# Optimization experiments

Hardware: AMD Instinct MI355X
Metric: run time of the kernel (lower is better)

The kernel has to match this reference:

```python
import jax, jax.numpy as jnp
import numpy as np

N_EMBED = 1024
HIDDEN = int(2 / 3 * 4 * N_EMBED)  # 2730, matches SwiGLU default
NUM_EXPERTS = 8
TOP_K = 2


def setup_inputs() -> dict:
    key = jax.random.key(0)
    ks = jax.random.split(key, 5)
    B, T, C, E, H = 2, 2048, N_EMBED, NUM_EXPERTS, HIDDEN
    s = 0.02
    return {
        "x": jax.random.normal(ks[0], (B, T, C), dtype=jnp.float32),
        "gate_w": jax.random.normal(ks[1], (E, C), dtype=jnp.float32) * s,  # Linear(C->E) weight [out,in]
        "w1": jax.random.normal(ks[2], (E, H, C), dtype=jnp.float32) * s,   # per-expert Linear(C->H)
        "w2": jax.random.normal(ks[3], (E, H, C), dtype=jnp.float32) * s,   # per-expert Linear(C->H)
        "w3": jax.random.normal(ks[4], (E, C, H), dtype=jnp.float32) * s,   # per-expert Linear(H->C)
    }


def reference(x, gate_w, w1, w2, w3):
    B, T, C = x.shape
    E = gate_w.shape[0]
    xt = x.reshape(-1, C)                      # [N, C], N = B*T
    N = xt.shape[0]

    # Router: top-k logits, softmax over the selected logits only
    logits = jnp.einsum("nc,ec->ne", xt, gate_w)          # [N, E]
    top_vals, top_idx = jax.lax.top_k(logits, TOP_K)       # [N, K]
    top_w = jax.nn.softmax(top_vals.astype(jnp.float32), axis=-1).astype(x.dtype)

    # Dense routing-weight matrix [N, E] (top-k indices are distinct per token)
    route = jnp.zeros((N, E), dtype=x.dtype)
    route = route.at[jnp.arange(N)[:, None], top_idx].set(top_w)

    # SwiGLU for all experts, batched over the expert axis (faithful math,
    # vectorized instead of the per-expert Python-loop gather/scatter)
    h1 = jnp.einsum("nc,ehc->enh", xt, w1)                 # [E, N, H]
    h2 = jnp.einsum("nc,ehc->enh", xt, w2)                 # [E, N, H]
    act = jax.nn.silu(h1) * h2                              # [E, N, H]
    expert_out = jnp.einsum("enh,ech->enc", act, w3)       # [E, N, C]

    out = jnp.einsum("ne,enc->nc", route, expert_out)      # weighted combine
    return out.reshape(B, T, C)
```

## Files before the change

### kernel.cpp

```cpp
#include <hip/hip_runtime.h>
#include <hip/hip_bf16.h>
#include <cstdint>
#include <cstddef>

#define TOKENS 4096
#define CDIM   1024
#define HDIM   2730
#define HPAD2  2816
#define NEXP   8
#define NPAIR  (TOKENS * 2)
#define NTB1   (HPAD2 / 128)
#define NTB2   (CDIM / 128)
#define NT1    (CDIM / 64)
#define NT2    (HPAD2 / 64)

typedef __bf16 bf16_t;
typedef bf16_t bf16x8 __attribute__((ext_vector_type(8)));
typedef float  f32x4  __attribute__((ext_vector_type(4)));

static __device__ __forceinline__ unsigned short f2bf(float f) {
    union { float f; unsigned int u; } v; v.f = f;
    unsigned int u = v.u;
    return (unsigned short)((u + 0x7FFFu + ((u >> 16) & 1u)) >> 16);
}
static __device__ __forceinline__ unsigned int pack2(float a, float b) {
    return (unsigned int)f2bf(a) | ((unsigned int)f2bf(b) << 16);
}

typedef __attribute__((address_space(3))) unsigned int lds_uint;
typedef const __attribute__((address_space(1))) unsigned int glob_uint;
static __device__ __forceinline__ void gl_lds16(const void* g, void* l) {
    __builtin_amdgcn_global_load_lds((glob_uint*)g, (lds_uint*)l, 16, 0, 0);
}


__global__ __launch_bounds__(256) void moe_zero(int* meta, float* out) {
    int b = blockIdx.x;
    float4 z4 = {0.f, 0.f, 0.f, 0.f};
#pragma unroll
    for (int i = 0; i < 4; ++i)
        ((float4*)out)[(size_t)b * 1024 + i * 256 + threadIdx.x] = z4;
    if (b == 0) {
        meta[threadIdx.x] = 0;
        meta[256 + threadIdx.x] = 0;
    }
}

__global__ __launch_bounds__(256) void moe_router(
    const float* __restrict__ x, const float* __restrict__ gw,
    int* __restrict__ meta, int* __restrict__ tok_idx, float* __restrict__ tok_w)
{
    int wave = threadIdx.x >> 6;
    int lane = threadIdx.x & 63;
    int t = blockIdx.x * 4 + wave;

    float acc[NEXP];
#pragma unroll
    for (int e = 0; e < NEXP; ++e) acc[e] = 0.f;

    const float4* xr = (const float4*)(x + (size_t)t * CDIM);
#pragma unroll
    for (int it = 0; it < 4; ++it) {
        int c4 = it * 64 + lane;
        float4 xv = xr[c4];
#pragma unroll
        for (int e = 0; e < NEXP; ++e) {
            float4 gv = ((const float4*)(gw + e * CDIM))[c4];
            acc[e] += xv.x * gv.x + xv.y * gv.y + xv.z * gv.z + xv.w * gv.w;
        }
    }
#pragma unroll
    for (int e = 0; e < NEXP; ++e) {
#pragma unroll
        for (int off = 32; off > 0; off >>= 1)
            acc[e] += __shfl_xor(acc[e], off, 64);
    }
    if (lane == 0) {
        int e0 = 0; float v0 = acc[0];
#pragma unroll
        for (int e = 1; e < NEXP; ++e) if (acc[e] > v0) { v0 = acc[e]; e0 = e; }
        int e1 = -1; float v1 = -3.0e38f;
#pragma unroll
        for (int e = 0; e < NEXP; ++e) if (e != e0 && acc[e] > v1) { v1 = acc[e]; e1 = e; }
        float w0 = 1.f / (1.f + __expf(v1 - v0));
        tok_idx[2 * t] = e0; tok_idx[2 * t + 1] = e1;
        tok_w[2 * t] = w0;  tok_w[2 * t + 1] = 1.f - w0;
        atomicAdd(&meta[e0], 1);
        atomicAdd(&meta[e1], 1);
    }
}

__global__ void moe_scan(int* meta) {
    if (threadIdx.x == 0) {
        int s = 0;
        for (int e = 0; e < NEXP; ++e) { meta[8 + e] = s; s += meta[e]; }
        meta[16] = s;
        int nb1 = 0;
        for (int e = 0; e < NEXP; ++e) {
            int beg = meta[8 + e], end = meta[8 + e] + meta[e];
            for (int m0 = beg; m0 < end; m0 += 256) {
                meta[32 + 2 * nb1] = e;
                meta[33 + 2 * nb1] = m0;
                ++nb1;
            }
        }
        meta[17] = nb1;
        int nb2 = 0;
        for (int e = 0; e < NEXP; ++e) {
            int beg = meta[8 + e], end = meta[8 + e] + meta[e];
            for (int m0 = beg; m0 < end; m0 += 128) {
                meta[128 + 2 * nb2] = e;
                meta[129 + 2 * nb2] = m0;
                ++nb2;
            }
        }
        meta[20] = nb2;
    }
}

__global__ __launch_bounds__(256) void moe_scatter(
    const int* __restrict__ tok_idx, const float* __restrict__ tok_w, int* meta,
    int* __restrict__ pair_token, float* __restrict__ pair_w)
{
    int t = blockIdx.x * 256 + threadIdx.x;
    if (t >= TOKENS) return;
#pragma unroll
    for (int k = 0; k < 2; ++k) {
        int e = tok_idx[2 * t + k];
        int pos = atomicAdd(&meta[24 + e], 1);
        int slot = meta[8 + e] + pos;
        pair_token[slot] = t;
        pair_w[slot] = tok_w[2 * t + k];
    }
}

__global__ __launch_bounds__(256) void moe_gather(
    const float* __restrict__ x, const int* __restrict__ pair_token,
    unsigned short* __restrict__ Xg)
{
    int base = blockIdx.x * 8;
    int i = threadIdx.x;
#pragma unroll
    for (int r = 0; r < 8; ++r) {
        int row = base + r;
        int t = pair_token[row];
        float4 v = ((const float4*)(x + (size_t)t * CDIM))[i];
        ushort4 o;
        o.x = f2bf(v.x); o.y = f2bf(v.y); o.z = f2bf(v.z); o.w = f2bf(v.w);
        ((ushort4*)(Xg + (size_t)row * CDIM))[i] = o;
    }
}

__global__ __launch_bounds__(256) void conv_all(
    const float* __restrict__ w1, const float* __restrict__ w2, const float* __restrict__ w3,
    unsigned short* __restrict__ w1b, unsigned short* __restrict__ w2b,
    unsigned short* __restrict__ w3b)
{
    int e = blockIdx.y;
    int z = blockIdx.z;
    if (z < 2) {
        const float* wsrc = z ? w2 : w1;
        unsigned short* wdst = z ? w2b : w1b;
        int half = threadIdx.x >> 7;
        int col = (threadIdx.x & 127) * 8;
#pragma unroll
        for (int r = 0; r < 4; ++r) {
            int row = blockIdx.x * 8 + r * 2 + half;
            unsigned short* dst = wdst + ((size_t)e * HPAD2 + row) * CDIM;
            uint4 pv;
            if (row < HDIM) {
                const float* src = wsrc + ((size_t)e * HDIM + row) * CDIM + col;
                float4 a = *(const float4*)(src);
                float4 b = *(const float4*)(src + 4);
                pv.x = pack2(a.x, a.y); pv.y = pack2(a.z, a.w);
                pv.z = pack2(b.x, b.y); pv.w = pack2(b.z, b.w);
            } else {
                pv = uint4{0, 0, 0, 0};
            }
            *(uint4*)(dst + col) = pv;
        }
    } else {
        if (blockIdx.x >= CDIM / 8) return;
#pragma unroll
        for (int r = 0; r < 8; ++r) {
            int row = blockIdx.x * 8 + r;
            const float* src = w3 + ((size_t)e * CDIM + row) * HDIM;
            unsigned short* dst = w3b + ((size_t)e * CDIM + row) * HPAD2;
            for (int ch = threadIdx.x; ch < HPAD2 / 8; ch += 256) {
                int h = ch * 8;
                uint4 pv;
                if (h + 8 <= HDIM) {
                    float2 a = *(const float2*)(src + h);
                    float2 b = *(const float2*)(src + h + 2);
                    float2 c = *(const float2*)(src + h + 4);
                    float2 d = *(const float2*)(src + h + 6);
                    pv.x = pack2(a.x, a.y); pv.y = pack2(b.x, b.y);
                    pv.z = pack2(c.x, c.y); pv.w = pack2(d.x, d.y);
                } else if (h < HDIM) {
                    float v[8];
#pragma unroll
                    for (int q = 0; q < 8; ++q) v[q] = (h + q < HDIM) ? src[h + q] : 0.f;
                    pv.x = pack2(v[0], v[1]); pv.y = pack2(v[2], v[3]);
                    pv.z = pack2(v[4], v[5]); pv.w = pack2(v[6], v[7]);
                } else {
                    pv = uint4{0, 0, 0, 0};
                }
                *(uint4*)(dst + h) = pv;
            }
        }
    }
}

#define SWZ(row, ch) (((row) << 6) + ((((ch) ^ ((row) & 7))) << 3))

__global__ __launch_bounds__(512, 2) void moe_gemm1(
    const unsigned short* __restrict__ Xg,
    const unsigned short* __restrict__ w1b, const unsigned short* __restrict__ w2b,
    const float* __restrict__ pair_w, int* __restrict__ meta,
    unsigned short* __restrict__ act)
{
    __shared__ unsigned short sA[2][256 * 64];
    __shared__ unsigned short sB[2][256 * 64];
    __shared__ int sTile;

    int tid = threadIdx.x;
    int lane = tid & 63;
    int wv = tid >> 6;
    int wm = wv >> 2, wn = wv & 3;
    int l3 = lane >> 3;
    int l15 = lane & 15, l4 = lane >> 4;
    int srcc = (((lane & 7) ^ l3) << 3);

    int ntile = meta[17] * NTB1;

    for (;;) {
        if (tid == 0) sTile = atomicAdd(&meta[18], 1);
        __syncthreads();
        int t = sTile;
        if (t >= ntile) break;

        int bm = t / NTB1, bn = t - bm * NTB1;
        int e  = meta[32 + 2 * bm];
        int m0 = meta[33 + 2 * bm];
        int mEnd = meta[9 + e];
        int mEndm1 = mEnd - 1;
        int n0 = bn * 128;

        const unsigned short* w1e = w1b + (size_t)e * HPAD2 * CDIM + (size_t)n0 * CDIM;
        const unsigned short* w2e = w2b + (size_t)e * HPAD2 * CDIM + (size_t)n0 * CDIM;
        const unsigned short* bbase = (wv < 4) ? w1e : w2e;

        f32x4 acc1[8][2], acc2[8][2];
#pragma unroll
        for (int i = 0; i < 8; ++i)
#pragma unroll
            for (int j = 0; j < 2; ++j) {
                acc1[i][j] = {0.f, 0.f, 0.f, 0.f};
                acc2[i][j] = {0.f, 0.f, 0.f, 0.f};
            }

        auto STAGE_A = [&](int b, int kk) {
            int k0 = kk * 64;
#pragma unroll
            for (int i_ = 0; i_ < 4; ++i_) {
                int seg = wv * 4 + i_;
                int arow = seg * 8 + l3;
                int grow = m0 + arow; if (grow > mEndm1) grow = mEndm1;
                gl_lds16(Xg + (size_t)grow * CDIM + k0 + srcc, sA[b] + seg * 512);
            }
        };
        auto STAGE_B = [&](int b, int kk) {
            int k0 = kk * 64;
#pragma unroll
            for (int i_ = 0; i_ < 4; ++i_) {
                int seg = wv * 4 + i_;
                int bseg = (wv < 4) ? seg : seg - 16;
                gl_lds16(bbase + (size_t)(bseg * 8 + l3) * CDIM + k0 + srcc, sB[b] + seg * 512);
            }
        };

        STAGE_A(0, 0); STAGE_B(0, 0);
        STAGE_A(1, 1); STAGE_B(1, 1);
        asm volatile("s_waitcnt vmcnt(8)" ::: "memory");
        __builtin_amdgcn_s_barrier();

        for (int t_ = 0; t_ < NT1; ++t_) {
            int cur = t_ & 1;
            const unsigned short* A = sA[cur];
            const unsigned short* B = sB[cur];
            bf16x8 af[2][4], b1f[2][2], b2f[2][2];

#pragma unroll
            for (int ks = 0; ks < 2; ++ks) {
                int kch = ks * 4 + l4;
#pragma unroll
                for (int i = 0; i < 4; ++i)
                    af[ks][i] = *(const bf16x8*)(A + SWZ(wm * 128 + i * 16 + l15, kch));
#pragma unroll
                for (int j = 0; j < 2; ++j)
                    b1f[ks][j] = *(const bf16x8*)(B + SWZ(wn * 32 + j * 16 + l15, kch));
            }
            __builtin_amdgcn_s_barrier();
            asm volatile("s_waitcnt lgkmcnt(0)" ::: "memory");
            __builtin_amdgcn_s_setprio(1);
#pragma unroll
            for (int ks = 0; ks < 2; ++ks)
#pragma unroll
                for (int i = 0; i < 4; ++i)
#pragma unroll
                    for (int j = 0; j < 2; ++j)
                        acc1[i][j] = __builtin_amdgcn_mfma_f32_16x16x32_bf16(af[ks][i], b1f[ks][j], acc1[i][j], 0, 0, 0);
            __builtin_amdgcn_s_setprio(0);
            __builtin_amdgcn_s_barrier();

#pragma unroll
            for (int ks = 0; ks < 2; ++ks) {
                int kch = ks * 4 + l4;
#pragma unroll
                for (int j = 0; j < 2; ++j)
                    b2f[ks][j] = *(const bf16x8*)(B + SWZ(128 + wn * 32 + j * 16 + l15, kch));
            }
            __builtin_amdgcn_s_barrier();
            asm volatile("s_waitcnt lgkmcnt(0)" ::: "memory");
            __builtin_amdgcn_s_setprio(1);
#pragma unroll
            for (int ks = 0; ks < 2; ++ks)
#pragma unroll
                for (int i = 0; i < 4; ++i)
#pragma unroll
                    for (int j = 0; j < 2; ++j)
                        acc2[i][j] = __builtin_amdgcn_mfma_f32_16x16x32_bf16(af[ks][i], b2f[ks][j], acc2[i][j], 0, 0, 0);
            __builtin_amdgcn_s_setprio(0);
            __builtin_amdgcn_s_barrier();

#pragma unroll
            for (int ks = 0; ks < 2; ++ks) {
                int kch = ks * 4 + l4;
#pragma unroll
                for (int i = 0; i < 4; ++i)
                    af[ks][i] = *(const bf16x8*)(A + SWZ(wm * 128 + 64 + i * 16 + l15, kch));
            }
            if (t_ + 2 < NT1) STAGE_B(cur, t_ + 2);
            __builtin_amdgcn_s_barrier();
            asm volatile("s_waitcnt lgkmcnt(0)" ::: "memory");
            __builtin_amdgcn_s_setprio(1);
#pragma unroll
            for (int ks = 0; ks < 2; ++ks)
#pragma unroll
                for (int i = 0; i < 4; ++i)
#pragma unroll
                    for (int j = 0; j < 2; ++j)
                        acc1[4 + i][j] = __builtin_amdgcn_mfma_f32_16x16x32_bf16(af[ks][i], b1f[ks][j], acc1[4 + i][j], 0, 0, 0);
            __builtin_amdgcn_s_setprio(0);
            __builtin_amdgcn_s_barrier();

            if (t_ + 2 < NT1) {
                STAGE_A(cur, t_ + 2);
                asm volatile("s_waitcnt vmcnt(8)" ::: "memory");
            } else {
                asm volatile("s_waitcnt vmcnt(0)" ::: "memory");
            }
            __builtin_amdgcn_s_barrier();
            __builtin_amdgcn_s_setprio(1);
#pragma unroll
            for (int ks = 0; ks < 2; ++ks)
#pragma unroll
                for (int i = 0; i < 4; ++i)
#pragma unroll
                    for (int j = 0; j < 2; ++j)
                        acc2[4 + i][j] = __builtin_amdgcn_mfma_f32_16x16x32_bf16(af[ks][i], b2f[ks][j], acc2[4 + i][j], 0, 0, 0);
            __builtin_amdgcn_s_setprio(0);
            __builtin_amdgcn_s_barrier();
        }

#pragma unroll
        for (int i = 0; i < 8; ++i) {
            int rbase = m0 + wm * 128 + ((i & 3) * 16) + ((i >> 2) * 64) + (l4 << 2);
#pragma unroll
            for (int r = 0; r < 4; ++r) {
                int grow = rbase + r;
                if (grow >= mEnd) continue;
                float pw = pair_w[grow];
                size_t rowoff = (size_t)grow * HPAD2;
#pragma unroll
                for (int j = 0; j < 2; ++j) {
                    int gcol = n0 + wn * 32 + j * 16 + l15;
                    int ai = (i & 3) + ((i >> 2) << 2);
                    float h1 = acc1[ai][j][r], h2 = acc2[ai][j][r];
                    float a = (h1 / (1.f + __expf(-h1))) * h2 * pw;
                    act[rowoff + gcol] = f2bf(a);
                }
            }
        }
    }
}

__global__ __launch_bounds__(512, 2) void moe_gemm2(
    const unsigned short* __restrict__ act,
    const unsigned short* __restrict__ w3b,
    int* __restrict__ meta, const int* __restrict__ pair_token,
    float* __restrict__ out)
{
    __shared__ unsigned short sA[2][128 * 64];
    __shared__ unsigned short sB[2][128 * 64];
    __shared__ int sTile;

    int tid = threadIdx.x;
    int lane = tid & 63;
    int wv = tid >> 6;
    int wm = wv >> 2, wn = wv & 3;
    int l3 = lane >> 3;
    int srcc = (((lane & 7) ^ l3) << 3);

    int ntile = meta[20] * NTB2;

    for (;;) {
        if (tid == 0) sTile = atomicAdd(&meta[19], 1);
        __syncthreads();
        int t = sTile;
        if (t >= ntile) break;

        int bm = t / NTB2, bn = t - bm * NTB2;
        int e  = meta[128 + 2 * bm];
        int m0 = meta[129 + 2 * bm];
        int mEnd = meta[9 + e];
        int mEndm1 = mEnd - 1;
        int n0 = bn * 128;

        const unsigned short* w3e = w3b + (size_t)e * CDIM * HPAD2 + (size_t)n0 * HPAD2;

        f32x4 acc[4][2];
#pragma unroll
        for (int i = 0; i < 4; ++i)
#pragma unroll
            for (int j = 0; j < 2; ++j) acc[i][j] = {0.f, 0.f, 0.f, 0.f};

        auto STAGE = [&](int b, int kk) {
            int k0 = kk * 64;
#pragma unroll
            for (int i_ = 0; i_ < 2; ++i_) {
                int seg = wv * 2 + i_;
                int row = seg * 8 + l3;
                int grow = m0 + row; if (grow > mEndm1) grow = mEndm1;
                gl_lds16(act + (size_t)grow * HPAD2 + k0 + srcc, sA[b] + seg * 512);
                gl_lds16(w3e + (size_t)row * HPAD2 + k0 + srcc, sB[b] + seg * 512);
            }
        };

        STAGE(0, 0);
        __syncthreads();
        for (int t_ = 0; t_ < NT2; ++t_) {
            int cur = t_ & 1;
            if (t_ + 1 < NT2) STAGE(cur ^ 1, t_ + 1);
#pragma unroll
            for (int ks = 0; ks < 2; ++ks) {
                int kch = ks * 4 + (lane >> 4);
                bf16x8 af[4], bf[2];
#pragma unroll
                for (int i = 0; i < 4; ++i) {
                    int r = wm * 64 + i * 16 + (lane & 15);
                    af[i] = *(const bf16x8*)(sA[cur] + SWZ(r, kch));
                }
#pragma unroll
                for (int j = 0; j < 2; ++j) {
                    int r = wn * 32 + j * 16 + (lane & 15);
                    bf[j] = *(const bf16x8*)(sB[cur] + SWZ(r, kch));
                }
#pragma unroll
                for (int i = 0; i < 4; ++i)
#pragma unroll
                    for (int j = 0; j < 2; ++j)
                        acc[i][j] = __builtin_amdgcn_mfma_f32_16x16x32_bf16(af[i], bf[j], acc[i][j], 0, 0, 0);
            }
            __syncthreads();
        }

#pragma unroll
        for (int i = 0; i < 4; ++i) {
            int rbase = m0 + wm * 64 + i * 16 + ((lane >> 4) << 2);
#pragma unroll
            for (int r = 0; r < 4; ++r) {
                int grow = rbase + r;
                if (grow >= mEnd) continue;
                int tok = pair_token[grow];
                float* orow = out + (size_t)tok * CDIM;
#pragma unroll
                for (int j = 0; j < 2; ++j) {
                    int gcol = n0 + wn * 32 + j * 16 + (lane & 15);
                    atomicAdd(orow + gcol, acc[i][j][r]);
                }
            }
        }
    }
}

extern "C" void kernel_launch(void* const* d_in, const int* in_sizes, int n_in,
                              void* d_out, int out_size, void* d_ws, size_t ws_size,
                              hipStream_t stream)
{
    const float* x  = (const float*)d_in[0];
    const float* gw = (const float*)d_in[1];
    const float* w1 = (const float*)d_in[2];
    const float* w2 = (const float*)d_in[3];
    const float* w3 = (const float*)d_in[4];
    float* out = (float*)d_out;

    char* ws = (char*)d_ws;
    size_t off = 0;
    auto alloc = [&](size_t bytes) -> void* {
        off = (off + 255) & ~(size_t)255;
        void* p = ws + off;
        off += bytes;
        return p;
    };
    int*   meta       = (int*)alloc(512 * sizeof(int));
    int*   tok_idx    = (int*)alloc((size_t)NPAIR * sizeof(int));
    float* tok_w      = (float*)alloc((size_t)NPAIR * sizeof(float));
    int*   pair_token = (int*)alloc((size_t)NPAIR * sizeof(int));
    float* pair_w     = (float*)alloc((size_t)NPAIR * sizeof(float));
    unsigned short* Xg  = (unsigned short*)alloc((size_t)NPAIR * CDIM * 2);
    unsigned short* act = (unsigned short*)alloc((size_t)NPAIR * HPAD2 * 2);
    unsigned short* w1b = (unsigned short*)alloc((size_t)NEXP * HPAD2 * CDIM * 2);
    unsigned short* w2b = (unsigned short*)alloc((size_t)NEXP * HPAD2 * CDIM * 2);
    unsigned short* w3b = (unsigned short*)alloc((size_t)NEXP * CDIM * HPAD2 * 2);
    (void)ws_size; (void)in_sizes; (void)n_in; (void)out_size;

    moe_zero<<<1024, 256, 0, stream>>>(meta, out);
    moe_router<<<TOKENS / 4, 256, 0, stream>>>(x, gw, meta, tok_idx, tok_w);
    moe_scan<<<1, 64, 0, stream>>>(meta);
    moe_scatter<<<TOKENS / 256, 256, 0, stream>>>(tok_idx, tok_w, meta, pair_token, pair_w);
    moe_gather<<<NPAIR / 8, 256, 0, stream>>>(x, pair_token, Xg);
    conv_all<<<dim3(HPAD2 / 8, NEXP, 3), 256, 0, stream>>>(w1, w2, w3, w1b, w2b, w3b);
    moe_gemm1<<<256, 512, 0, stream>>>(Xg, w1b, w2b, pair_w, meta, act);
    moe_gemm2<<<512, 512, 0, stream>>>(act, w3b, meta, pair_token, out);
}
```

Before: 507.8 us.

## Fuse prep kernels, overlap w3 conversion into gemm1, split gemm2 K in halves

Folds zeroing of the output into the router launch, merges the token gather with the w1/w2 bf16 conversion, and moves the w3 conversion into the tail of gemm1's persistent tile queue. This removes several launches and their serialization. gemm2 now splits the K dimension into two halves per tile, doubling tile count to improve load balance across CUs, which relies on atomic accumulation into the output. The cost is extra atomic traffic in gemm2, and w3 conversion blocks compete with gemm1 tiles for the same workers.

```diff
diff --git a/kernel.cpp b/kernel.cpp
--- a/kernel.cpp
+++ b/kernel.cpp
@@ -12,7 +12,8 @@
 #define NTB1   (HPAD2 / 128)
 #define NTB2   (CDIM / 128)
 #define NT1    (CDIM / 64)
-#define NT2    (HPAD2 / 64)
+#define NT2H   (HPAD2 / 2 / 64)
+#define NCONV3 256
 
 typedef __bf16 bf16_t;
 typedef bf16_t bf16x8 __attribute__((ext_vector_type(8)));
@@ -34,22 +35,19 @@
 }
 
 
-__global__ __launch_bounds__(256) void moe_zero(int* meta, float* out) {
-    int b = blockIdx.x;
-    float4 z4 = {0.f, 0.f, 0.f, 0.f};
-#pragma unroll
-    for (int i = 0; i < 4; ++i)
-        ((float4*)out)[(size_t)b * 1024 + i * 256 + threadIdx.x] = z4;
-    if (b == 0) {
-        meta[threadIdx.x] = 0;
-        meta[256 + threadIdx.x] = 0;
-    }
-}
-
-__global__ __launch_bounds__(256) void moe_router(
+__global__ __launch_bounds__(256) void moe_router_zero(
     const float* __restrict__ x, const float* __restrict__ gw,
-    int* __restrict__ meta, int* __restrict__ tok_idx, float* __restrict__ tok_w)
+    int* __restrict__ meta, int* __restrict__ tok_idx, float* __restrict__ tok_w,
+    float* __restrict__ out)
 {
+    if (blockIdx.x >= 1024) {
+        int b = blockIdx.x - 1024;
+        float4 z4 = {0.f, 0.f, 0.f, 0.f};
+#pragma unroll
+        for (int i = 0; i < 4; ++i)
+            ((float4*)out)[(size_t)b * 1024 + i * 256 + threadIdx.x] = z4;
+        return;
+    }
     int wave = threadIdx.x >> 6;
     int lane = threadIdx.x & 63;
     int t = blockIdx.x * 4 + wave;
@@ -134,68 +132,99 @@
     }
 }
 
-__global__ __launch_bounds__(256) void moe_gather(
+__global__ __launch_bounds__(256) void moe_gather_conv12(
     const float* __restrict__ x, const int* __restrict__ pair_token,
-    unsigned short* __restrict__ Xg)
+    unsigned short* __restrict__ Xg,
+    const float* __restrict__ w1, const float* __restrict__ w2,
+    unsigned short* __restrict__ w1b, unsigned short* __restrict__ w2b)
 {
-    int base = blockIdx.x * 8;
-    int i = threadIdx.x;
-#pragma unroll
-    for (int r = 0; r < 8; ++r) {
-        int row = base + r;
-        int t = pair_token[row];
-        float4 v = ((const float4*)(x + (size_t)t * CDIM))[i];
-        ushort4 o;
-        o.x = f2bf(v.x); o.y = f2bf(v.y); o.z = f2bf(v.z); o.w = f2bf(v.w);
-        ((ushort4*)(Xg + (size_t)row * CDIM))[i] = o;
-    }
-}
-
-__global__ __launch_bounds__(256) void conv_all(
-    const float* __restrict__ w1, const float* __restrict__ w2, const float* __restrict__ w3,
-    unsigned short* __restrict__ w1b, unsigned short* __restrict__ w2b,
-    unsigned short* __restrict__ w3b)
+    if (blockIdx.x < 1024) {
+        int base = blockIdx.x * 8;
+        int i = threadIdx.x;
+#pragma unroll
+        for (int r = 0; r < 8; ++r) {
+            int row = base + r;
+            int t = pair_token[row];
+            float4 v = ((const float4*)(x + (size_t)t * CDIM))[i];
+            ushort4 o;
+            o.x = f2bf(v.x); o.y = f2bf(v.y); o.z = f2bf(v.z); o.w = f2bf(v.w);
+            ((ushort4*)(Xg + (size_t)row * CDIM))[i] = o;
+        }
+        return;
+    }
+    int zz = blockIdx.x - 1024;
+    int which = zz / 2816;
+    int rr = zz - which * 2816;
+    int e = rr / 352;
+    int blk = rr - e * 352;
+    const float* wsrc = which ? w2 : w1;
+    unsigned short* wdst = which ? w2b : w1b;
+    int half = threadIdx.x >> 7;
+    int col = (threadIdx.x & 127) * 8;
+#pragma unroll
+    for (int r = 0; r < 4; ++r) {
+        int row = blk * 8 + r * 2 + half;
+        unsigned short* dst = wdst + ((size_t)e * HPAD2 + row) * CDIM;
+        uint4 pv;
+        if (row < HDIM) {
+            const float* src = wsrc + ((size_t)e * HDIM + row) * CDIM + col;
+            float4 a = *(const float4*)(src);
+            float4 b = *(const float4*)(src + 4);
+            pv.x = pack2(a.x, a.y); pv.y = pack2(a.z, a.w);
+            pv.z = pack2(b.x, b.y); pv.w = pack2(b.z, b.w);
+        } else {
+            pv = uint4{0, 0, 0, 0};
+        }
+        *(uint4*)(dst + col) = pv;
+    }
+}
+
+#define SWZ(row, ch) (((row) << 6) + ((((ch) ^ ((row) & 7))) << 3))
+
+__global__ __launch_bounds__(512, 2) void moe_gemm1(
+    const unsigned short* __restrict__ Xg,
+    const unsigned short* __restrict__ w1b, const unsigned short* __restrict__ w2b,
+    const float* __restrict__ pair_w, int* __restrict__ meta,
+    unsigned short* __restrict__ act,
+    const float* __restrict__ w3, unsigned short* __restrict__ w3b)
 {
-    int e = blockIdx.y;
-    int z = blockIdx.z;
-    if (z < 2) {
-        const float* wsrc = z ? w2 : w1;
-        unsigned short* wdst = z ? w2b : w1b;
-        int half = threadIdx.x >> 7;
-        int col = (threadIdx.x & 127) * 8;
-#pragma unroll
-        for (int r = 0; r < 4; ++r) {
-            int row = blockIdx.x * 8 + r * 2 + half;
-            unsigned short* dst = wdst + ((size_t)e * HPAD2 + row) * CDIM;
-            uint4 pv;
-            if (row < HDIM) {
-                const float* src = wsrc + ((size_t)e * HDIM + row) * CDIM + col;
-                float4 a = *(const float4*)(src);
-                float4 b = *(const float4*)(src + 4);
-                pv.x = pack2(a.x, a.y); pv.y = pack2(a.z, a.w);
-                pv.z = pack2(b.x, b.y); pv.w = pack2(b.z, b.w);
-            } else {
-                pv = uint4{0, 0, 0, 0};
-            }
-            *(uint4*)(dst + col) = pv;
-        }
-    } else {
-        if (blockIdx.x >= CDIM / 8) return;
-#pragma unroll
-        for (int r = 0; r < 8; ++r) {
-            int row = blockIdx.x * 8 + r;
-            const float* src = w3 + ((size_t)e * CDIM + row) * HDIM;
-            unsigned short* dst = w3b + ((size_t)e * CDIM + row) * HPAD2;
-            for (int ch = threadIdx.x; ch < HPAD2 / 8; ch += 256) {
-                int h = ch * 8;
+    __shared__ unsigned short sA[2][256 * 64];
+    __shared__ unsigned short sB[2][256 * 64];
+    __shared__ int sTile;
+
+    int tid = threadIdx.x;
+    int lane = tid & 63;
+    int wv = tid >> 6;
+    int wm = wv >> 2, wn = wv & 3;
+    int l3 = lane >> 3;
+    int l15 = lane & 15, l4 = lane >> 4;
+    int srcc = (((lane & 7) ^ l3) << 3);
+
+    int ntile = meta[17] * NTB1;
+
+    for (;;) {
+        if (tid == 0) sTile = atomicAdd(&meta[18], 1);
+        __syncthreads();
+        int t = sTile;
+        if (t >= ntile + NCONV3) break;
+
+        if (t >= ntile) {
+            int c = t - ntile;
+            int grow = c * 32 + (tid >> 4);
+            int lanec = tid & 15;
+            const float* src = w3 + (size_t)grow * HDIM;
+            unsigned short* dst = w3b + (size_t)grow * HPAD2;
+#pragma unroll
+            for (int k = 0; k < 22; ++k) {
+                int h = (lanec + k * 16) * 8;
                 uint4 pv;
                 if (h + 8 <= HDIM) {
                     float2 a = *(const float2*)(src + h);
                     float2 b = *(const float2*)(src + h + 2);
-                    float2 c = *(const float2*)(src + h + 4);
+                    float2 c2 = *(const float2*)(src + h + 4);
                     float2 d = *(const float2*)(src + h + 6);
                     pv.x = pack2(a.x, a.y); pv.y = pack2(b.x, b.y);
-                    pv.z = pack2(c.x, c.y); pv.w = pack2(d.x, d.y);
+                    pv.z = pack2(c2.x, c2.y); pv.w = pack2(d.x, d.y);
                 } else if (h < HDIM) {
                     float v[8];
 #pragma unroll
@@ -207,37 +236,8 @@
                 }
                 *(uint4*)(dst + h) = pv;
             }
-        }
-    }
-}
-
-#define SWZ(row, ch) (((row) << 6) + ((((ch) ^ ((row) & 7))) << 3))
-
-__global__ __launch_bounds__(512, 2) void moe_gemm1(
-    const unsigned short* __restrict__ Xg,
-    const unsigned short* __restrict__ w1b, const unsigned short* __restrict__ w2b,
-    const float* __restrict__ pair_w, int* __restrict__ meta,
-    unsigned short* __restrict__ act)
-{
-    __shared__ unsigned short sA[2][256 * 64];
-    __shared__ unsigned short sB[2][256 * 64];
-    __shared__ int sTile;
-
-    int tid = threadIdx.x;
-    int lane = tid & 63;
-    int wv = tid >> 6;
-    int wm = wv >> 2, wn = wv & 3;
-    int l3 = lane >> 3;
-    int l15 = lane & 15, l4 = lane >> 4;
-    int srcc = (((lane & 7) ^ l3) << 3);
-
-    int ntile = meta[17] * NTB1;
-
-    for (;;) {
-        if (tid == 0) sTile = atomicAdd(&meta[18], 1);
-        __syncthreads();
-        int t = sTile;
-        if (t >= ntile) break;
+            continue;
+        }
 
         int bm = t / NTB1, bn = t - bm * NTB1;
         int e  = meta[32 + 2 * bm];
@@ -412,7 +412,7 @@
     int l3 = lane >> 3;
     int srcc = (((lane & 7) ^ l3) << 3);
 
-    int ntile = meta[20] * NTB2;
+    int ntile = meta[20] * NTB2 * 2;
 
     for (;;) {
         if (tid == 0) sTile = atomicAdd(&meta[19], 1);
@@ -420,12 +420,16 @@
         int t = sTile;
         if (t >= ntile) break;
 
-        int bm = t / NTB2, bn = t - bm * NTB2;
+        int bm = t >> 4;
+        int rem = t & 15;
+        int bn = rem >> 1;
+        int kh = rem & 1;
         int e  = meta[128 + 2 * bm];
         int m0 = meta[129 + 2 * bm];
         int mEnd = meta[9 + e];
         int mEndm1 = mEnd - 1;
         int n0 = bn * 128;
+        int kbase = kh * (HPAD2 / 2);
 
         const unsigned short* w3e = w3b + (size_t)e * CDIM * HPAD2 + (size_t)n0 * HPAD2;
 
@@ -436,7 +440,7 @@
             for (int j = 0; j < 2; ++j) acc[i][j] = {0.f, 0.f, 0.f, 0.f};
 
         auto STAGE = [&](int b, int kk) {
-            int k0 = kk * 64;
+            int k0 = kbase + kk * 64;
 #pragma unroll
             for (int i_ = 0; i_ < 2; ++i_) {
                 int seg = wv * 2 + i_;
@@ -449,9 +453,9 @@
 
         STAGE(0, 0);
         __syncthreads();
-        for (int t_ = 0; t_ < NT2; ++t_) {
+        for (int t_ = 0; t_ < NT2H; ++t_) {
             int cur = t_ & 1;
-            if (t_ + 1 < NT2) STAGE(cur ^ 1, t_ + 1);
+            if (t_ + 1 < NT2H) STAGE(cur ^ 1, t_ + 1);
 #pragma unroll
             for (int ks = 0; ks < 2; ++ks) {
                 int kch = ks * 4 + (lane >> 4);
@@ -525,12 +529,11 @@
     unsigned short* w3b = (unsigned short*)alloc((size_t)NEXP * CDIM * HPAD2 * 2);
     (void)ws_size; (void)in_sizes; (void)n_in; (void)out_size;
 
-    moe_zero<<<1024, 256, 0, stream>>>(meta, out);
-    moe_router<<<TOKENS / 4, 256, 0, stream>>>(x, gw, meta, tok_idx, tok_w);
+    hipMemsetAsync(meta, 0, 512 * sizeof(int), stream);
+    moe_router_zero<<<2048, 256, 0, stream>>>(x, gw, meta, tok_idx, tok_w, out);
     moe_scan<<<1, 64, 0, stream>>>(meta);
     moe_scatter<<<TOKENS / 256, 256, 0, stream>>>(tok_idx, tok_w, meta, pair_token, pair_w);
-    moe_gather<<<NPAIR / 8, 256, 0, stream>>>(x, pair_token, Xg);
-    conv_all<<<dim3(HPAD2 / 8, NEXP, 3), 256, 0, stream>>>(w1, w2, w3, w1b, w2b, w3b);
-    moe_gemm1<<<256, 512, 0, stream>>>(Xg, w1b, w2b, pair_w, meta, act);
+    moe_gather_conv12<<<1024 + 5632, 256, 0, stream>>>(x, pair_token, Xg, w1, w2, w1b, w2b);
+    moe_gemm1<<<256, 512, 0, stream>>>(Xg, w1b, w2b, pair_w, meta, act, w3, w3b);
     moe_gemm2<<<512, 512, 0, stream>>>(act, w3b, meta, pair_token, out);
 }
```

New measurement: 526.6 us. +3.7%, slower.
